# Performance work log

Hardware: AMD Instinct MI355X
Metric: run time of the kernel (lower is better)

The kernel has to match this reference:

```python
import jax, jax.numpy as jnp
import numpy as np

B, N, C = 8, 2048, 64  # batch, num nodes, channels
DENSITY = 0.01


def setup_inputs() -> dict:
    key = jax.random.key(0)
    k = jax.random.split(key, 8)
    x = jax.random.normal(k[0], (B, N, C), dtype=jnp.float32)

    # --- replicate sym_norm_Adj(Adj_matrix) + row softmax from __init__ ---
    W = (jax.random.uniform(k[1], (N, N)) < DENSITY).astype(jnp.float32)
    W = W + 0.5 * jnp.eye(N, dtype=jnp.float32)          # W + 0.5*I
    deg = jnp.sum((W != 0.0).astype(jnp.float32), axis=1)  # row nonzero counts
    A = jnp.sqrt(deg)[:, None] * W * jnp.sqrt(deg)[None, :]  # sqrt(D) W sqrt(D)
    A = jax.nn.softmax(A, axis=1)

    s = 1.0 / np.sqrt(C)
    Wq = jax.random.normal(k[2], (C, C), dtype=jnp.float32) * s   # stored as (in,out)
    Wk = jax.random.normal(k[3], (C, C), dtype=jnp.float32) * s
    Wv = jax.random.normal(k[4], (C, N), dtype=jnp.float32) * s   # c_in -> num_node
    theta_w = jax.random.normal(k[5], (C, C), dtype=jnp.float32) * s
    theta_b = jnp.zeros((C,), dtype=jnp.float32)
    alpha = jnp.array([0.95], dtype=jnp.float32)
    beta = jnp.array([0.95], dtype=jnp.float32)
    return {"x": x, "A": A, "Wq": Wq, "Wk": Wk, "Wv": Wv,
            "theta_w": theta_w, "theta_b": theta_b, "alpha": alpha, "beta": beta}


def reference(x, A, Wq, Wk, Wv, theta_w, theta_b, alpha, beta):
    # Spatial_Attention_layer
    Q = x @ Wq                                   # (B,N,C)
    K = x @ Wk                                   # (B,N,C)
    V = x @ Wv                                   # (B,N,N)
    score = jnp.einsum('bnc,bmc->bnm', Q, K)     # (B,N,N)
    score = jax.nn.softmax(score, axis=1)        # softmax over dim=1 (as in torch code)
    spat = jnp.einsum('bnm,bmk->bnk', score, V)  # (B,N,N) spatial attention

    # einsum('nn,bnc->bnc', A, x) == diag(A) broadcast-multiply
    static_out = jnp.diagonal(A)[None, :, None] * x  # (B,N,C)

    # dy_adj = A @ spat; einsum('bnn,bnc->bnc', dy_adj, x) uses only diag(dy_adj)
    dy_diag = jnp.einsum('nj,bjn->bn', A, spat)      # (B,N), avoids (B,N,N) intermediate
    dy_out = (dy_diag[:, :, None] * x) @ theta_w + theta_b  # Theta1 linear

    out = jax.nn.relu(alpha[0] * static_out + beta[0] * dy_out)
    return out
```

## Files before the change

kernel.cpp:

```cpp
#include <hip/hip_runtime.h>

constexpr int Bb = 8;
constexpr int Nn = 2048;
constexpr int Cc = 64;
constexpr int CAPS = 192;

typedef __attribute__((ext_vector_type(4))) float f32x4;
typedef __attribute__((ext_vector_type(16))) float f32x16;
typedef __attribute__((ext_vector_type(8))) short bf16x8;
typedef __attribute__((ext_vector_type(4))) unsigned u32x4;

__device__ inline unsigned short f2bf(float f){
  unsigned u = __builtin_bit_cast(unsigned, f);
  unsigned r = (u + 0x7FFFu + ((u>>16)&1u)) >> 16;
  return (unsigned short)r;
}
__device__ inline float bf2f(unsigned short h){
  unsigned u = ((unsigned)h)<<16; return __builtin_bit_cast(float,u);
}
__device__ inline unsigned pk2(float a, float b){
  return (unsigned)f2bf(a) | ((unsigned)f2bf(b)<<16);
}

__device__ inline size_t qk_chunk(int b, int s, int q, int l){
  return ((((size_t)b*64 + s)*4 + q)*64 + l)*8;
}
__device__ inline size_t xz_chunk(int b, int mq, int cb, int l){
  return ((((size_t)b*128 + mq)*2 + cb)*64 + l)*8;
}

#define MFMA32(a,b,c) __builtin_amdgcn_mfma_f32_32x32x16_bf16(a,b,c,0,0,0)

__global__ __launch_bounds__(256) void mega_k(
    const float* __restrict__ x, const float* __restrict__ A,
    const float* __restrict__ Wq, const float* __restrict__ Wk,
    const float* __restrict__ Tw, const float* __restrict__ Wv,
    unsigned short* __restrict__ Qhi, unsigned short* __restrict__ Qlo,
    unsigned short* __restrict__ Khi, unsigned short* __restrict__ Klo,
    float* __restrict__ xt, float* __restrict__ Xp,
    float* __restrict__ r_, float* __restrict__ diagA, int* __restrict__ cnt,
    int* __restrict__ idx, float* __restrict__ val,
    float* __restrict__ WvT){
  __shared__ __attribute__((aligned(16))) char smem[65792];
  int blk = blockIdx.x; int t = threadIdx.x;

  if(blk < 256){
    float* wql = (float*)smem;
    float* wkl = wql + 4096;
    float* twl = wkl + 4096;
    float (*xr)[64] = (float(*)[64])(twl + 4096);
    float* xsl = (float*)(xr + 64);
    #pragma unroll
    for(int i=0;i<4;i++){
      *(f32x4*)&wql[i*1024+t*4] = *(const f32x4*)&Wq[i*1024+t*4];
      *(f32x4*)&wkl[i*1024+t*4] = *(const f32x4*)&Wk[i*1024+t*4];
      *(f32x4*)&twl[i*1024+t*4] = *(const f32x4*)&Tw[i*1024+t*4];
    }
    if(t<64) xsl[t]=0.f;
    long long row0 = (long long)blk*64;
    int r = t>>4, q = t&15, c0 = q*4;
    #pragma unroll
    for(int i=0;i<4;i++){
      int row = i*16 + r;
      *(f32x4*)&xr[row][c0] = *(const f32x4*)&x[(row0+row)*Cc + c0];
    }
    __syncthreads();
    f32x4 aq[4], ak[4], at4[4];
    #pragma unroll
    for(int g=0;g<4;g++){ aq[g]=(f32x4){0,0,0,0}; ak[g]=(f32x4){0,0,0,0}; at4[g]=(f32x4){0,0,0,0}; }
    for(int kk=0;kk<64;kk++){
      f32x4 wq4 = *(const f32x4*)&wql[kk*64+c0];
      f32x4 wk4 = *(const f32x4*)&wkl[kk*64+c0];
      f32x4 wt4 = *(const f32x4*)&twl[kk*64+c0];
      #pragma unroll
      for(int g=0;g<4;g++){
        float xv = xr[g*16+r][kk];
        aq[g] += xv*wq4; ak[g] += xv*wk4; at4[g] += xv*wt4;
      }
    }
    float xsp[4] = {0.f,0.f,0.f,0.f};
    int q2 = c0>>4, hb = (c0>>3)&1, cs = c0&7;
    #pragma unroll
    for(int g=0;g<4;g++){
      #pragma unroll
      for(int d=0;d<4;d++) xsp[d] += xr[g*16+r][c0+d];
      long long rg = row0 + g*16 + r;
      unsigned long long hq=0,lq=0,hk=0,lk=0;
      #pragma unroll
      for(int d=0;d<4;d++){
        float v = aq[g][d];
        unsigned short h = f2bf(v); unsigned short lo2 = f2bf(v - bf2f(h));
        hq |= (unsigned long long)h << (16*d); lq |= (unsigned long long)lo2 << (16*d);
        v = ak[g][d];
        h = f2bf(v); lo2 = f2bf(v - bf2f(h));
        hk |= (unsigned long long)h << (16*d); lk |= (unsigned long long)lo2 << (16*d);
      }
      int b2 = (int)(rg>>11); int s2 = ((int)rg>>5)&63;
      int l2 = ((int)rg&31) + 32*hb;
      size_t off = qk_chunk(b2, s2, q2, l2) + cs;
      *(unsigned long long*)&Qhi[off] = hq;
      *(unsigned long long*)&Qlo[off] = lq;
      *(unsigned long long*)&Khi[off] = hk;
      *(unsigned long long*)&Klo[off] = lk;
      *(f32x4*)&xt[rg*Cc + c0] = at4[g];
    }
    __syncthreads();
    #pragma unroll
    for(int d=0;d<4;d++) atomicAdd(&xsl[c0+d], xsp[d]);
    __syncthreads();
    if(t<64) Xp[blk*64+t] = xsl[t];
  } else if(blk < 768){
    int n = (blk-256)*4 + (t>>6); int l = t&63;
    const float* row = A + (size_t)n*Nn;
    float mn = 1e30f;
    for(int j=l;j<Nn;j+=64) mn = fminf(mn, row[j]);
    #pragma unroll
    for(int off=32;off>=1;off>>=1) mn = fminf(mn, __shfl_xor(mn,off));
    float thr = mn*1.3f;
    int bse=0;
    for(int j0=0;j0<Nn;j0+=64){
      float v = row[j0+l];
      bool f = v>thr;
      unsigned long long m = __ballot(f);
      int pos = __popcll(m & ((1ull<<l)-1ull));
      if(f && bse+pos<CAPS){ idx[n*CAPS+bse+pos]=j0+l; val[n*CAPS+bse+pos]=v-mn; }
      bse += __popcll(m);
    }
    if(l==0){ r_[n]=mn; diagA[n]=row[n]; cnt[n] = bse<CAPS? bse : CAPS; }
  } else {
    float (*tile)[65] = (float(*)[65])smem;
    int n0 = (blk-768)*64;
    for(int i=0;i<16;i++){
      int cc = i*4 + (t>>6); int nn2 = t&63;
      tile[cc][nn2] = Wv[(size_t)cc*Nn + n0 + nn2];
    }
    __syncthreads();
    for(int i=0;i<16;i++){
      int nn2 = i*4 + (t>>6); int cc = t&63;
      WvT[(size_t)(n0+nn2)*Cc + cc] = tile[cc][nn2];
    }
  }
}

__global__ __launch_bounds__(256,2) void zpass_k(
    const unsigned short* __restrict__ Qhi, const unsigned short* __restrict__ Qlo,
    const unsigned short* __restrict__ Khi, const unsigned short* __restrict__ Klo,
    float* __restrict__ Z){
  __shared__ float Zl[32];
  int id = blockIdx.x; int b = id&7; int mt = id>>3;
  int t = threadIdx.x, w = t>>6, l = t&63;
  if(t<32) Zl[t]=0.f;
  __syncthreads();
  bf16x8 Kh[4], Kl4[4];
  #pragma unroll
  for(int q=0;q<4;q++){
    Kh[q]  = *(const bf16x8*)(Khi + qk_chunk(b, mt, q, l));
    Kl4[q] = *(const bf16x8*)(Klo + qk_chunk(b, mt, q, l));
  }
  float zacc = 0.f;
  for(int jt=0; jt<16; jt++){
    int s = w*16 + jt;
    bf16x8 Qh4[4], Ql4[4];
    #pragma unroll
    for(int q=0;q<4;q++){
      Qh4[q] = *(const bf16x8*)(Qhi + qk_chunk(b, s, q, l));
      Ql4[q] = *(const bf16x8*)(Qlo + qk_chunk(b, s, q, l));
    }
    f32x16 sa;
    #pragma unroll
    for(int r=0;r<16;r++) sa[r]=0.f;
    #pragma unroll
    for(int q=0;q<4;q++){
      sa = MFMA32(Qh4[q], Kh[q],  sa);
      sa = MFMA32(Ql4[q], Kh[q],  sa);
      sa = MFMA32(Qh4[q], Kl4[q], sa);
    }
    float p = 0.f;
    #pragma unroll
    for(int r=0;r<16;r++) p += __expf(sa[r]);
    zacc += p;
  }
  zacc += __shfl_down(zacc, 32);
  if(l<32) atomicAdd(&Zl[l], zacc);
  __syncthreads();
  if(t<32) Z[(size_t)b*Nn + mt*32 + t] = Zl[t];
}

__global__ __launch_bounds__(256) void xzt_k(const float* __restrict__ x,
    const float* __restrict__ Z, unsigned short* __restrict__ xzf){
  __shared__ float tile[64][65];
  __shared__ float izl[64];
  int id = blockIdx.x; int b = id&7; int mt = id>>3;
  int m0 = mt*64; int t = threadIdx.x;
  for(int i=0;i<16;i++){
    int mm = i*4 + (t>>6); int cc = t&63;
    tile[mm][cc] = x[((size_t)b*Nn + m0+mm)*Cc + cc];
  }
  if(t<64) izl[t] = 1.0f/Z[(size_t)b*Nn + m0 + t];
  __syncthreads();
  #pragma unroll
  for(int i=0;i<2;i++){
    int k2 = i*256 + t; int mg = k2>>6; int c = k2&63;
    int mloc = mg*8;
    unsigned u0 = pk2(tile[mloc+0][c]*izl[mloc+0], tile[mloc+1][c]*izl[mloc+1]);
    unsigned u1 = pk2(tile[mloc+2][c]*izl[mloc+2], tile[mloc+3][c]*izl[mloc+3]);
    unsigned u2 = pk2(tile[mloc+4][c]*izl[mloc+4], tile[mloc+5][c]*izl[mloc+5]);
    unsigned u3 = pk2(tile[mloc+6][c]*izl[mloc+6], tile[mloc+7][c]*izl[mloc+7]);
    u32x4 uu = {u0,u1,u2,u3};
    int mq = (m0 + mloc)>>4; int cb = c>>5; int l2 = (c&31) + 32*(mg&1);
    *(u32x4*)(xzf + xz_chunk(b, mq, cb, l2)) = uu;
  }
}

__global__ __launch_bounds__(256,2) void fused_k(
    const unsigned short* __restrict__ Qhi, const unsigned short* __restrict__ Qlo,
    const unsigned short* __restrict__ Khi, const unsigned short* __restrict__ Klo,
    const unsigned short* __restrict__ xzf, float* __restrict__ P){
  __shared__ float plds[32*64];
  int id = blockIdx.x; int b = id&7; int js = id>>3;
  int t = threadIdx.x, w = t>>6, l = t&63, lr = l&31, hh = l>>5;
  #pragma unroll
  for(int i=0;i<8;i++) plds[i*256+t]=0.f;
  __syncthreads();
  bf16x8 Qh4[4], Ql4[4];
  #pragma unroll
  for(int q=0;q<4;q++){
    Qh4[q] = *(const bf16x8*)(Qhi + qk_chunk(b, js, q, l));
    Ql4[q] = *(const bf16x8*)(Qlo + qk_chunk(b, js, q, l));
  }
  f32x16 pa0, pa1;
  #pragma unroll
  for(int r=0;r<16;r++){ pa0[r]=0.f; pa1[r]=0.f; }
  for(int mt=0; mt<16; mt++){
    int s = w*16 + mt;
    bf16x8 Kh4[4], Kl4[4];
    #pragma unroll
    for(int q=0;q<4;q++){
      Kh4[q] = *(const bf16x8*)(Khi + qk_chunk(b, s, q, l));
      Kl4[q] = *(const bf16x8*)(Klo + qk_chunk(b, s, q, l));
    }
    int mq = s*2;
    bf16x8 b00 = *(const bf16x8*)(xzf + xz_chunk(b, mq,   0, l));
    bf16x8 b01 = *(const bf16x8*)(xzf + xz_chunk(b, mq+1, 0, l));
    bf16x8 b10 = *(const bf16x8*)(xzf + xz_chunk(b, mq,   1, l));
    bf16x8 b11 = *(const bf16x8*)(xzf + xz_chunk(b, mq+1, 1, l));
    f32x16 sa;
    #pragma unroll
    for(int r=0;r<16;r++) sa[r]=0.f;
    #pragma unroll
    for(int q=0;q<4;q++){
      sa = MFMA32(Kh4[q], Qh4[q], sa);
      sa = MFMA32(Kl4[q], Qh4[q], sa);
      sa = MFMA32(Kh4[q], Ql4[q], sa);
    }
    unsigned wd0,wd1,wd2,wd3,wd4,wd5,wd6,wd7;
    {
      unsigned x0 = pk2(__expf(sa[0]),  __expf(sa[1]));
      unsigned x1 = pk2(__expf(sa[2]),  __expf(sa[3]));
      unsigned y0 = pk2(__expf(sa[4]),  __expf(sa[5]));
      unsigned y1 = pk2(__expf(sa[6]),  __expf(sa[7]));
      asm("v_permlane32_swap_b32 %0, %1" : "+v"(x0), "+v"(y0));
      asm("v_permlane32_swap_b32 %0, %1" : "+v"(x1), "+v"(y1));
      wd0=x0; wd1=x1; wd2=y0; wd3=y1;
      unsigned x2 = pk2(__expf(sa[8]),  __expf(sa[9]));
      unsigned x3 = pk2(__expf(sa[10]), __expf(sa[11]));
      unsigned y2 = pk2(__expf(sa[12]), __expf(sa[13]));
      unsigned y3 = pk2(__expf(sa[14]), __expf(sa[15]));
      asm("v_permlane32_swap_b32 %0, %1" : "+v"(x2), "+v"(y2));
      asm("v_permlane32_swap_b32 %0, %1" : "+v"(x3), "+v"(y3));
      wd4=x2; wd5=x3; wd6=y2; wd7=y3;
    }
    u32x4 u1 = {wd0,wd1,wd2,wd3};
    u32x4 u2 = {wd4,wd5,wd6,wd7};
    bf16x8 f1 = __builtin_bit_cast(bf16x8, u1);
    bf16x8 f2 = __builtin_bit_cast(bf16x8, u2);
    pa0 = MFMA32(f1, b00, pa0);
    pa0 = MFMA32(f2, b01, pa0);
    pa1 = MFMA32(f1, b10, pa1);
    pa1 = MFMA32(f2, b11, pa1);
  }
  #pragma unroll
  for(int r=0;r<16;r++){
    int jr = (r&3) + 8*(r>>2) + 4*hh;
    atomicAdd(&plds[jr*64 + lr],      pa0[r]);
    atomicAdd(&plds[jr*64 + 32 + lr], pa1[r]);
  }
  __syncthreads();
  {
    int j = t>>3, c0 = (t&7)*8;
    float* Pb = P + ((size_t)b*Nn + js*32 + j)*Cc + c0;
    *(f32x4*)Pb     = *(const f32x4*)&plds[j*64 + c0];
    *(f32x4*)(Pb+4) = *(const f32x4*)&plds[j*64 + c0 + 4];
  }
}

__global__ __launch_bounds__(256) void final_k(const float* __restrict__ x,
    const float* __restrict__ xt, const float* __restrict__ P,
    const float* __restrict__ WvT, const float* __restrict__ Xp,
    const float* __restrict__ r_, const float* __restrict__ diagA,
    const int* __restrict__ cnt, const int* __restrict__ idx,
    const float* __restrict__ val, const float* __restrict__ tb,
    const float* __restrict__ alp, const float* __restrict__ bet,
    float* __restrict__ out){
  int t=threadIdx.x; int l=t&63;
  int bn = blockIdx.x*4 + (t>>6);
  int b = bn>>11, n = bn&2047;
  float wv = WvT[n*Cc+l];
  float xs = 0.f;
  const float* xpb = Xp + (size_t)b*32*Cc;
  #pragma unroll 8
  for(int p=0;p<32;p++) xs += xpb[p*Cc + l];
  float tacc = r_[n]*xs;
  int cn = cnt[n];
  const float* Pb = P + (size_t)b*Nn*Cc;
  const int* ix = idx + n*CAPS;
  const float* vl = val + n*CAPS;
  for(int k=0;k<cn;k++)
    tacc += vl[k] * Pb[(size_t)ix[k]*Cc + l];
  float d = wv*tacc;
  #pragma unroll
  for(int off=32;off>=1;off>>=1) d += __shfl_xor(d,off);
  size_t g = (size_t)bn*Cc + l;
  float o = alp[0]*diagA[n]*x[g] + bet[0]*(d*xt[g] + tb[l]);
  out[g] = fmaxf(o,0.f);
}

extern "C" void kernel_launch(void* const* d_in, const int* in_sizes, int n_in,
                              void* d_out, int out_size, void* d_ws, size_t ws_size,
                              hipStream_t stream){
  const float* x  = (const float*)d_in[0];
  const float* A  = (const float*)d_in[1];
  const float* Wq = (const float*)d_in[2];
  const float* Wk = (const float*)d_in[3];
  const float* Wv = (const float*)d_in[4];
  const float* Tw = (const float*)d_in[5];
  const float* tb = (const float*)d_in[6];
  const float* alp= (const float*)d_in[7];
  const float* bet= (const float*)d_in[8];
  float* out = (float*)d_out;

  char* base = (char*)d_ws; size_t off=0;
  auto al=[&](size_t sz)->void*{ void* q = base+off; off=(off+sz+255)&~(size_t)255; return q; };
  unsigned short* Qhi=(unsigned short*)al((size_t)Bb*Nn*Cc*2);
  unsigned short* Qlo=(unsigned short*)al((size_t)Bb*Nn*Cc*2);
  unsigned short* Khi=(unsigned short*)al((size_t)Bb*Nn*Cc*2);
  unsigned short* Klo=(unsigned short*)al((size_t)Bb*Nn*Cc*2);
  float* xt  =(float*)al((size_t)Bb*Nn*Cc*4);
  float* P   =(float*)al((size_t)Bb*Nn*Cc*4);
  float* Z   =(float*)al((size_t)Bb*Nn*4);
  float* Xp  =(float*)al((size_t)256*Cc*4);
  float* WvT =(float*)al((size_t)Nn*Cc*4);
  float* r_  =(float*)al((size_t)Nn*4);
  float* dgA =(float*)al((size_t)Nn*4);
  int*   cnt =(int*)al((size_t)Nn*4);
  int*   idx =(int*)al((size_t)Nn*CAPS*4);
  float* val =(float*)al((size_t)Nn*CAPS*4);
  unsigned short* xzf=(unsigned short*)al((size_t)Bb*Cc*Nn*2);
  (void)ws_size;

  mega_k<<<800, 256, 0, stream>>>(x, A, Wq, Wk, Tw, Wv,
      Qhi, Qlo, Khi, Klo, xt, Xp, r_, dgA, cnt, idx, val, WvT);
  zpass_k<<<512, 256, 0, stream>>>(Qhi,Qlo,Khi,Klo,Z);
  xzt_k<<<256, 256, 0, stream>>>(x,Z,xzf);
  fused_k<<<512, 256, 0, stream>>>(Qhi,Qlo,Khi,Klo,xzf,P);
  final_k<<<Bb*Nn/4, 256, 0, stream>>>(x,xt,P,WvT,Xp,r_,dgA,cnt,idx,val,tb,alp,bet,out);
}
```

Baseline: 131.7 us.

## Split zpass and fused kernels along reduction dimension with partial buffers

Splits the softmax-normalizer pass four ways and the attention-times-xz pass two ways along the reduction axis. Each split writes partial sums to separate buffers, which xzt_k and final_k then add. This gives 2048 and 1024 blocks instead of 512, filling the 256 CUs better. It also splits each MFMA accumulation chain into two independent accumulators to hide MFMA latency. The cost is extra partial-buffer traffic, a second P read per gathered row in final_k, and re-reading Q in the fused kernel per split.

```diff
diff --git a/kernel.cpp b/kernel.cpp
--- a/kernel.cpp
+++ b/kernel.cpp
@@ -142,12 +142,13 @@
   }
 }
 
-__global__ __launch_bounds__(256,2) void zpass_k(
+__global__ __launch_bounds__(256,4) void zpass_k(
     const unsigned short* __restrict__ Qhi, const unsigned short* __restrict__ Qlo,
     const unsigned short* __restrict__ Khi, const unsigned short* __restrict__ Klo,
-    float* __restrict__ Z){
+    float* __restrict__ Zp){
   __shared__ float Zl[32];
-  int id = blockIdx.x; int b = id&7; int mt = id>>3;
+  int id = blockIdx.x;
+  int b = id&7; int mt = (id>>3)&63; int jq = id>>9;
   int t = threadIdx.x, w = t>>6, l = t&63;
   if(t<32) Zl[t]=0.f;
   __syncthreads();
@@ -158,36 +159,37 @@
     Kl4[q] = *(const bf16x8*)(Klo + qk_chunk(b, mt, q, l));
   }
   float zacc = 0.f;
-  for(int jt=0; jt<16; jt++){
-    int s = w*16 + jt;
+  #pragma unroll
+  for(int jt=0; jt<4; jt++){
+    int s = jq*16 + w*4 + jt;
     bf16x8 Qh4[4], Ql4[4];
     #pragma unroll
     for(int q=0;q<4;q++){
       Qh4[q] = *(const bf16x8*)(Qhi + qk_chunk(b, s, q, l));
       Ql4[q] = *(const bf16x8*)(Qlo + qk_chunk(b, s, q, l));
     }
-    f32x16 sa;
-    #pragma unroll
-    for(int r=0;r<16;r++) sa[r]=0.f;
+    f32x16 sa, sb;
+    #pragma unroll
+    for(int r=0;r<16;r++){ sa[r]=0.f; sb[r]=0.f; }
     #pragma unroll
     for(int q=0;q<4;q++){
       sa = MFMA32(Qh4[q], Kh[q],  sa);
-      sa = MFMA32(Ql4[q], Kh[q],  sa);
-      sa = MFMA32(Qh4[q], Kl4[q], sa);
+      sb = MFMA32(Ql4[q], Kh[q],  sb);
+      sb = MFMA32(Qh4[q], Kl4[q], sb);
     }
     float p = 0.f;
     #pragma unroll
-    for(int r=0;r<16;r++) p += __expf(sa[r]);
+    for(int r=0;r<16;r++) p += __expf(sa[r]+sb[r]);
     zacc += p;
   }
   zacc += __shfl_down(zacc, 32);
   if(l<32) atomicAdd(&Zl[l], zacc);
   __syncthreads();
-  if(t<32) Z[(size_t)b*Nn + mt*32 + t] = Zl[t];
+  if(t<32) Zp[((size_t)(jq*8 + b))*Nn + mt*32 + t] = Zl[t];
 }
 
 __global__ __launch_bounds__(256) void xzt_k(const float* __restrict__ x,
-    const float* __restrict__ Z, unsigned short* __restrict__ xzf){
+    const float* __restrict__ Zp, unsigned short* __restrict__ xzf){
   __shared__ float tile[64][65];
   __shared__ float izl[64];
   int id = blockIdx.x; int b = id&7; int mt = id>>3;
@@ -196,7 +198,12 @@
     int mm = i*4 + (t>>6); int cc = t&63;
     tile[mm][cc] = x[((size_t)b*Nn + m0+mm)*Cc + cc];
   }
-  if(t<64) izl[t] = 1.0f/Z[(size_t)b*Nn + m0 + t];
+  if(t<64){
+    float z = 0.f;
+    #pragma unroll
+    for(int jq=0;jq<4;jq++) z += Zp[((size_t)(jq*8 + b))*Nn + m0 + t];
+    izl[t] = 1.0f/z;
+  }
   __syncthreads();
   #pragma unroll
   for(int i=0;i<2;i++){
@@ -212,12 +219,13 @@
   }
 }
 
-__global__ __launch_bounds__(256,2) void fused_k(
+__global__ __launch_bounds__(256,3) void fused_k(
     const unsigned short* __restrict__ Qhi, const unsigned short* __restrict__ Qlo,
     const unsigned short* __restrict__ Khi, const unsigned short* __restrict__ Klo,
-    const unsigned short* __restrict__ xzf, float* __restrict__ P){
+    const unsigned short* __restrict__ xzf, float* __restrict__ Pp){
   __shared__ float plds[32*64];
-  int id = blockIdx.x; int b = id&7; int js = id>>3;
+  int id = blockIdx.x;
+  int b = id&7; int js = (id>>3)&63; int mh = id>>9;
   int t = threadIdx.x, w = t>>6, l = t&63, lr = l&31, hh = l>>5;
   #pragma unroll
   for(int i=0;i<8;i++) plds[i*256+t]=0.f;
@@ -231,8 +239,8 @@
   f32x16 pa0, pa1;
   #pragma unroll
   for(int r=0;r<16;r++){ pa0[r]=0.f; pa1[r]=0.f; }
-  for(int mt=0; mt<16; mt++){
-    int s = w*16 + mt;
+  for(int mt=0; mt<8; mt++){
+    int s = mh*32 + w*8 + mt;
     bf16x8 Kh4[4], Kl4[4];
     #pragma unroll
     for(int q=0;q<4;q++){
@@ -244,28 +252,28 @@
     bf16x8 b01 = *(const bf16x8*)(xzf + xz_chunk(b, mq+1, 0, l));
     bf16x8 b10 = *(const bf16x8*)(xzf + xz_chunk(b, mq,   1, l));
     bf16x8 b11 = *(const bf16x8*)(xzf + xz_chunk(b, mq+1, 1, l));
-    f32x16 sa;
-    #pragma unroll
-    for(int r=0;r<16;r++) sa[r]=0.f;
+    f32x16 sa, sb;
+    #pragma unroll
+    for(int r=0;r<16;r++){ sa[r]=0.f; sb[r]=0.f; }
     #pragma unroll
     for(int q=0;q<4;q++){
       sa = MFMA32(Kh4[q], Qh4[q], sa);
-      sa = MFMA32(Kl4[q], Qh4[q], sa);
-      sa = MFMA32(Kh4[q], Ql4[q], sa);
+      sb = MFMA32(Kl4[q], Qh4[q], sb);
+      sb = MFMA32(Kh4[q], Ql4[q], sb);
     }
     unsigned wd0,wd1,wd2,wd3,wd4,wd5,wd6,wd7;
     {
-      unsigned x0 = pk2(__expf(sa[0]),  __expf(sa[1]));
-      unsigned x1 = pk2(__expf(sa[2]),  __expf(sa[3]));
-      unsigned y0 = pk2(__expf(sa[4]),  __expf(sa[5]));
-      unsigned y1 = pk2(__expf(sa[6]),  __expf(sa[7]));
+      unsigned x0 = pk2(__expf(sa[0]+sb[0]),   __expf(sa[1]+sb[1]));
+      unsigned x1 = pk2(__expf(sa[2]+sb[2]),   __expf(sa[3]+sb[3]));
+      unsigned y0 = pk2(__expf(sa[4]+sb[4]),   __expf(sa[5]+sb[5]));
+      unsigned y1 = pk2(__expf(sa[6]+sb[6]),   __expf(sa[7]+sb[7]));
       asm("v_permlane32_swap_b32 %0, %1" : "+v"(x0), "+v"(y0));
       asm("v_permlane32_swap_b32 %0, %1" : "+v"(x1), "+v"(y1));
       wd0=x0; wd1=x1; wd2=y0; wd3=y1;
-      unsigned x2 = pk2(__expf(sa[8]),  __expf(sa[9]));
-      unsigned x3 = pk2(__expf(sa[10]), __expf(sa[11]));
-      unsigned y2 = pk2(__expf(sa[12]), __expf(sa[13]));
-      unsigned y3 = pk2(__expf(sa[14]), __expf(sa[15]));
+      unsigned x2 = pk2(__expf(sa[8]+sb[8]),   __expf(sa[9]+sb[9]));
+      unsigned x3 = pk2(__expf(sa[10]+sb[10]), __expf(sa[11]+sb[11]));
+      unsigned y2 = pk2(__expf(sa[12]+sb[12]), __expf(sa[13]+sb[13]));
+      unsigned y3 = pk2(__expf(sa[14]+sb[14]), __expf(sa[15]+sb[15]));
       asm("v_permlane32_swap_b32 %0, %1" : "+v"(x2), "+v"(y2));
       asm("v_permlane32_swap_b32 %0, %1" : "+v"(x3), "+v"(y3));
       wd4=x2; wd5=x3; wd6=y2; wd7=y3;
@@ -287,15 +295,15 @@
   }
   __syncthreads();
   {
+    float* Pb = Pp + (size_t)mh*Bb*Nn*Cc + ((size_t)b*Nn + js*32)*Cc;
     int j = t>>3, c0 = (t&7)*8;
-    float* Pb = P + ((size_t)b*Nn + js*32 + j)*Cc + c0;
-    *(f32x4*)Pb     = *(const f32x4*)&plds[j*64 + c0];
-    *(f32x4*)(Pb+4) = *(const f32x4*)&plds[j*64 + c0 + 4];
+    *(f32x4*)(Pb + (size_t)j*Cc + c0)     = *(const f32x4*)&plds[j*64 + c0];
+    *(f32x4*)(Pb + (size_t)j*Cc + c0 + 4) = *(const f32x4*)&plds[j*64 + c0 + 4];
   }
 }
 
 __global__ __launch_bounds__(256) void final_k(const float* __restrict__ x,
-    const float* __restrict__ xt, const float* __restrict__ P,
+    const float* __restrict__ xt, const float* __restrict__ Pp,
     const float* __restrict__ WvT, const float* __restrict__ Xp,
     const float* __restrict__ r_, const float* __restrict__ diagA,
     const int* __restrict__ cnt, const int* __restrict__ idx,
@@ -312,11 +320,14 @@
   for(int p=0;p<32;p++) xs += xpb[p*Cc + l];
   float tacc = r_[n]*xs;
   int cn = cnt[n];
-  const float* Pb = P + (size_t)b*Nn*Cc;
+  const float* Pb0 = Pp + (size_t)b*Nn*Cc;
+  const float* Pb1 = Pp + (size_t)Bb*Nn*Cc + (size_t)b*Nn*Cc;
   const int* ix = idx + n*CAPS;
   const float* vl = val + n*CAPS;
-  for(int k=0;k<cn;k++)
-    tacc += vl[k] * Pb[(size_t)ix[k]*Cc + l];
+  for(int k=0;k<cn;k++){
+    size_t ro = (size_t)ix[k]*Cc + l;
+    tacc += vl[k] * (Pb0[ro] + Pb1[ro]);
+  }
   float d = wv*tacc;
   #pragma unroll
   for(int off=32;off>=1;off>>=1) d += __shfl_xor(d,off);
@@ -346,8 +357,8 @@
   unsigned short* Khi=(unsigned short*)al((size_t)Bb*Nn*Cc*2);
   unsigned short* Klo=(unsigned short*)al((size_t)Bb*Nn*Cc*2);
   float* xt  =(float*)al((size_t)Bb*Nn*Cc*4);
-  float* P   =(float*)al((size_t)Bb*Nn*Cc*4);
-  float* Z   =(float*)al((size_t)Bb*Nn*4);
+  float* Pp  =(float*)al((size_t)2*Bb*Nn*Cc*4);
+  float* Zp  =(float*)al((size_t)4*Bb*Nn*4);
   float* Xp  =(float*)al((size_t)256*Cc*4);
   float* WvT =(float*)al((size_t)Nn*Cc*4);
   float* r_  =(float*)al((size_t)Nn*4);
@@ -360,8 +371,8 @@
 
   mega_k<<<800, 256, 0, stream>>>(x, A, Wq, Wk, Tw, Wv,
       Qhi, Qlo, Khi, Klo, xt, Xp, r_, dgA, cnt, idx, val, WvT);
-  zpass_k<<<512, 256, 0, stream>>>(Qhi,Qlo,Khi,Klo,Z);
-  xzt_k<<<256, 256, 0, stream>>>(x,Z,xzf);
-  fused_k<<<512, 256, 0, stream>>>(Qhi,Qlo,Khi,Klo,xzf,P);
-  final_k<<<Bb*Nn/4, 256, 0, stream>>>(x,xt,P,WvT,Xp,r_,dgA,cnt,idx,val,tb,alp,bet,out);
-}
+  zpass_k<<<2048, 256, 0, stream>>>(Qhi,Qlo,Khi,Klo,Zp);
+  xzt_k<<<256, 256, 0, stream>>>(x,Zp,xzf);
+  fused_k<<<1024, 256, 0, stream>>>(Qhi,Qlo,Khi,Klo,xzf,Pp);
+  final_k<<<Bb*Nn/4, 256, 0, stream>>>(x,xt,Pp,WvT,Xp,r_,dgA,cnt,idx,val,tb,alp,bet,out);
+}
```

New measurement: 144.7 us. 1.1x slower.
